# Performance work log

Measured on AMD Instinct MI355X. Metric: run time of the kernel, lower is better.

The kernel has to match this reference:

```python
import jax, jax.numpy as jnp
import numpy as np

B, L, D_MODEL, COND = 2, 2048, 1024, 1024
D_STATE, EXPAND = 64, 2
D_INNER = EXPAND * D_MODEL
MLP_H = 2 * D_MODEL  # mlp_expansion=2
EPS = 1e-5


def setup_inputs() -> dict:
    key = jax.random.key(0)
    ks = jax.random.split(key, 24)
    p = lambda i, shape, s=0.02: (jax.random.normal(ks[i], shape, jnp.float32) * s)
    inp = {
        "x": jax.random.normal(ks[0], (B, L, D_MODEL), jnp.float32),
        "c": jax.random.normal(ks[1], (B, COND), jnp.float32),
        "adaln_mamba_w": p(2, (COND, 3 * D_MODEL)),
        "adaln_mamba_b": jnp.zeros((3 * D_MODEL,), jnp.float32),
        "adaln_mlp_w": p(3, (COND, 3 * D_MODEL)),
        "adaln_mlp_b": jnp.zeros((3 * D_MODEL,), jnp.float32),
        "mlp_w1": p(4, (D_MODEL, MLP_H)),
        "mlp_w2": p(5, (D_MODEL, MLP_H)),
        "mlp_w3": p(6, (MLP_H, D_MODEL)),
    }
    a_init = jnp.log(jnp.tile(jnp.arange(1, D_STATE + 1, dtype=jnp.float32), (D_INNER, 1)))
    for j, pre in enumerate(["fwd", "bwd"]):
        o = 7 + 6 * j
        inp[f"{pre}_in_w"] = p(o, (D_MODEL, 2 * D_INNER))
        inp[f"{pre}_xproj_w"] = p(o + 1, (D_INNER, D_INNER + 2 * D_STATE))
        inp[f"{pre}_dt_bias"] = jnp.zeros((D_INNER,), jnp.float32)
        inp[f"{pre}_A_log"] = a_init
        inp[f"{pre}_D"] = jnp.ones((D_INNER,), jnp.float32)
        inp[f"{pre}_out_w"] = p(o + 2, (D_INNER, D_MODEL))
    return inp


def _adaln(x, c, w, b):
    mod = (c @ w + b)[:, None, :]  # (B,1,3D)
    shift, scale, gate = jnp.split(mod, 3, axis=-1)
    mu = jnp.mean(x, axis=-1, keepdims=True)
    var = jnp.var(x, axis=-1, keepdims=True)
    normed = (x - mu) * jax.lax.rsqrt(var + EPS) * (1.0 + scale) + shift
    return normed, gate


def _ssm(h, in_w, xproj_w, dt_bias, A_log, Dskip, out_w):
    """Selective-SSM: h (B,L,D) -> (B,L,D)."""
    xz = h @ in_w                      # (B,L,2*di)
    xs, z = jnp.split(xz, 2, axis=-1)
    xs = jax.nn.silu(xs)               # (B,L,di)
    proj = xs @ xproj_w                # (B,L,di+2*ds)
    dt = jax.nn.softplus(proj[..., :D_INNER] + dt_bias)        # (B,L,di)
    Bm = proj[..., D_INNER:D_INNER + D_STATE]                  # (B,L,ds)
    Cm = proj[..., D_INNER + D_STATE:]                         # (B,L,ds)
    A = -jnp.exp(A_log)                                        # (di,ds)

    def step(hst, ins):
        dt_t, B_t, C_t, x_t = ins  # (B,di),(B,ds),(B,ds),(B,di)
        dA = jnp.exp(dt_t[:, :, None] * A)                     # (B,di,ds)
        hst = hst * dA + (dt_t * x_t)[:, :, None] * B_t[:, None, :]
        y_t = jnp.einsum('bds,bs->bd', hst, C_t)
        return hst, y_t

    tm = lambda a: jnp.swapaxes(a, 0, 1)  # time-major
    h0 = jnp.zeros((h.shape[0], D_INNER, D_STATE), h.dtype)
    _, ys = jax.lax.scan(step, h0, (tm(dt), tm(Bm), tm(Cm), tm(xs)))
    y = jnp.swapaxes(ys, 0, 1) + xs * Dskip
    return (y * jax.nn.silu(z)) @ out_w


def reference(x, c, adaln_mamba_w, adaln_mamba_b, adaln_mlp_w, adaln_mlp_b,
              mlp_w1, mlp_w2, mlp_w3,
              fwd_in_w, fwd_xproj_w, fwd_dt_bias, fwd_A_log, fwd_D, fwd_out_w,
              bwd_in_w, bwd_xproj_w, bwd_dt_bias, bwd_A_log, bwd_D, bwd_out_w):
    h, gate = _adaln(x, c, adaln_mamba_w, adaln_mamba_b)
    h_fwd = _ssm(h, fwd_in_w, fwd_xproj_w, fwd_dt_bias, fwd_A_log, fwd_D, fwd_out_w)
    h_bwd = jnp.flip(_ssm(jnp.flip(h, 1), bwd_in_w, bwd_xproj_w, bwd_dt_bias, bwd_A_log, bwd_D, bwd_out_w), 1)
    x = x + gate * (h_fwd + h_bwd)
    h, gate = _adaln(x, c, adaln_mlp_w, adaln_mlp_b)
    mlp_out = (jax.nn.silu(h @ mlp_w1) * (h @ mlp_w2)) @ mlp_w3
    return x + gate * mlp_out
```

## Files before the change

### kernel.cpp

```cpp
#include <hip/hip_runtime.h>
#include <hip/hip_bf16.h>
#include <math.h>

#define B_SZ 2
#define LSEQ 2048
#define DM   1024
#define DI   2048
#define NTOK (B_SZ*LSEQ)
#define EPSV 1e-5f

typedef __attribute__((ext_vector_type(8))) short short8v;
typedef __attribute__((ext_vector_type(4))) short short4v;
typedef __attribute__((ext_vector_type(4))) float f4v;

static __device__ __forceinline__ float sigmoidf_(float v) {
    return 1.f / (1.f + __expf(-v));
}
static __device__ __forceinline__ float softplus_(float v) {
    return fmaxf(v, 0.f) + log1pf(__expf(-fabsf(v)));
}
static __device__ __forceinline__ short f2bf(float f) {
    __hip_bfloat16 h = __float2bfloat16(f);
    return *reinterpret_cast<short*>(&h);
}
static __device__ __forceinline__ float bf2f(short s) {
    union { unsigned u; float f; } c;
    c.u = ((unsigned)(unsigned short)s) << 16;
    return c.f;
}

__global__ __launch_bounds__(256) void mod_kernel(const float* __restrict__ c,
                                                  const float* __restrict__ w,
                                                  const float* __restrict__ bias,
                                                  float* __restrict__ mod) {
    int jt = blockIdx.x * 32;
    int jj = threadIdx.x & 31, ks = threadIdx.x >> 5;
    int j = jt + jj;
    const float* c0 = c;
    const float* c1 = c + 1024;
    float a0 = 0.f, a1 = 0.f;
    int k0 = ks * 128;
#pragma unroll 4
    for (int k = k0; k < k0 + 128; ++k) {
        float wv = w[(size_t)k * 3072 + j];
        a0 = fmaf(c0[k], wv, a0);
        a1 = fmaf(c1[k], wv, a1);
    }
    __shared__ float red[2][8][32];
    red[0][ks][jj] = a0;
    red[1][ks][jj] = a1;
    __syncthreads();
    if (threadIdx.x < 64) {
        int bb = threadIdx.x >> 5, j2 = threadIdx.x & 31;
        float s = bias[jt + j2];
#pragma unroll
        for (int kk = 0; kk < 8; ++kk) s += red[bb][kk][j2];
        mod[bb * 3072 + jt + j2] = s;
    }
}

__global__ __launch_bounds__(256) void adaln_kernel(const float* __restrict__ x,
                                                    const float* __restrict__ mod,
                                                    __hip_bfloat16* __restrict__ h) {
    int row = blockIdx.x;
    int b = row >> 11;
    const float* xr = x + (size_t)row * DM;
    float v[4], s = 0.f, s2 = 0.f;
#pragma unroll
    for (int i = 0; i < 4; ++i) {
        v[i] = xr[threadIdx.x + i * 256];
        s += v[i]; s2 += v[i] * v[i];
    }
#pragma unroll
    for (int off = 32; off; off >>= 1) { s += __shfl_xor(s, off); s2 += __shfl_xor(s2, off); }
    __shared__ float red[8];
    int wid = threadIdx.x >> 6;
    if ((threadIdx.x & 63) == 0) { red[wid] = s; red[4 + wid] = s2; }
    __syncthreads();
    s  = red[0] + red[1] + red[2] + red[3];
    s2 = red[4] + red[5] + red[6] + red[7];
    float mu  = s * (1.f / DM);
    float var = s2 * (1.f / DM) - mu * mu;
    float rstd = rsqrtf(var + EPSV);
    const float* mb = mod + b * 3072;
    __hip_bfloat16* hr = h + (size_t)row * DM;
#pragma unroll
    for (int i = 0; i < 4; ++i) {
        int d = threadIdx.x + i * 256;
        hr[d] = __float2bfloat16((v[i] - mu) * rstd * (1.f + mb[1024 + d]) + mb[d]);
    }
}

template <int ACCUM>
__global__ __launch_bounds__(256) void gemm_bf16_kernel(
    const short* __restrict__ A, int lda,
    const short* __restrict__ Bt, int ldb,
    float* __restrict__ C, int ldc, int K)
{
    __shared__ short As[128][40];
    __shared__ short Bs[128][40];
    int tid = threadIdx.x;
    int m0 = blockIdx.y * 128, n0 = blockIdx.x * 128;
    int wave = tid >> 6, lane = tid & 63;
    int wm = (wave & 1) * 64, wn = (wave >> 1) * 64;
    int srow = tid >> 2, sq = (tid & 3) * 8;
    const short* aptr = A + (size_t)(m0 + srow) * lda + sq;
    const short* bptr = Bt + (size_t)(n0 + srow) * ldb + sq;
    int fr = lane & 15, fq = lane >> 4;
    f4v acc[4][4];
#pragma unroll
    for (int i = 0; i < 4; ++i)
#pragma unroll
        for (int j = 0; j < 4; ++j) acc[i][j] = (f4v){0.f, 0.f, 0.f, 0.f};

    short8v a0 = *(const short8v*)(aptr);
    short8v a1 = *(const short8v*)(aptr + 64 * (size_t)lda);
    short8v b0 = *(const short8v*)(bptr);
    short8v b1 = *(const short8v*)(bptr + 64 * (size_t)ldb);
    for (int k0 = 0; k0 < K; k0 += 32) {
        __syncthreads();
        *(short8v*)&As[srow][sq]      = a0;
        *(short8v*)&As[srow + 64][sq] = a1;
        *(short8v*)&Bs[srow][sq]      = b0;
        *(short8v*)&Bs[srow + 64][sq] = b1;
        __syncthreads();
        if (k0 + 32 < K) {
            a0 = *(const short8v*)(aptr + k0 + 32);
            a1 = *(const short8v*)(aptr + 64 * (size_t)lda + k0 + 32);
            b0 = *(const short8v*)(bptr + k0 + 32);
            b1 = *(const short8v*)(bptr + 64 * (size_t)ldb + k0 + 32);
        }
        short8v af[4], bf[4];
#pragma unroll
        for (int i = 0; i < 4; ++i) af[i] = *(const short8v*)&As[wm + i * 16 + fr][fq * 8];
#pragma unroll
        for (int j = 0; j < 4; ++j) bf[j] = *(const short8v*)&Bs[wn + j * 16 + fr][fq * 8];
#pragma unroll
        for (int i = 0; i < 4; ++i)
#pragma unroll
            for (int j = 0; j < 4; ++j)
                acc[i][j] = __builtin_amdgcn_mfma_f32_16x16x32_bf16(af[i], bf[j], acc[i][j], 0, 0, 0);
    }
#pragma unroll
    for (int i = 0; i < 4; ++i)
#pragma unroll
        for (int j = 0; j < 4; ++j) {
#pragma unroll
            for (int r = 0; r < 4; ++r) {
                int row = m0 + wm + i * 16 + fq * 4 + r;
                int col = n0 + wn + j * 16 + fr;
                float* cp = C + (size_t)row * ldc + col;
                if (ACCUM) *cp += acc[i][j][r]; else *cp = acc[i][j][r];
            }
        }
}

__global__ __launch_bounds__(256) void wcast_kernel(const float* __restrict__ w,
                                                    int K, int N,
                                                    short* __restrict__ wT) {
    __shared__ short tile[32][33];
    int c0 = blockIdx.x * 32, r0 = blockIdx.y * 32;
    int tx = threadIdx.x & 31, ty = threadIdx.x >> 5;
#pragma unroll
    for (int i = 0; i < 32; i += 8)
        tile[ty + i][tx] = f2bf(w[(size_t)(r0 + ty + i) * N + c0 + tx]);
    __syncthreads();
#pragma unroll
    for (int i = 0; i < 32; i += 8)
        wT[(size_t)(c0 + ty + i) * K + r0 + tx] = tile[tx][ty + i];
}

__global__ void silu_xs_kernel(float* __restrict__ xz, __hip_bfloat16* __restrict__ xsb) {
    int idx = blockIdx.x * 256 + threadIdx.x;
    int row = idx >> 9, c = (idx & 511) << 2;
    float4* p = (float4*)(xz + (size_t)row * 4096 + c);
    float4 v = *p;
    v.x *= sigmoidf_(v.x); v.y *= sigmoidf_(v.y);
    v.z *= sigmoidf_(v.z); v.w *= sigmoidf_(v.w);
    *p = v;
    short4v s = {f2bf(v.x), f2bf(v.y), f2bf(v.z), f2bf(v.w)};
    *(short4v*)((short*)xsb + (size_t)row * 2048 + c) = s;
}

__global__ __launch_bounds__(256) void transpose_inplace_kernel(float* __restrict__ M) {
    int bj = blockIdx.x, bi = blockIdx.y;
    if (bi > bj) return;
    __shared__ float ta[32][33], tb[32][33];
    int tx = threadIdx.x & 31, ty = threadIdx.x >> 5;
    size_t oA = ((size_t)bi * 32) * 4096 + (size_t)bj * 32;
    size_t oB = ((size_t)bj * 32) * 4096 + (size_t)bi * 32;
#pragma unroll
    for (int i = 0; i < 32; i += 8)
        ta[ty + i][tx] = M[oA + (size_t)(ty + i) * 4096 + tx];
    if (bi != bj) {
#pragma unroll
        for (int i = 0; i < 32; i += 8)
            tb[ty + i][tx] = M[oB + (size_t)(ty + i) * 4096 + tx];
    }
    __syncthreads();
#pragma unroll
    for (int i = 0; i < 32; i += 8)
        M[oB + (size_t)(ty + i) * 4096 + tx] = ta[tx][ty + i];
    if (bi != bj) {
#pragma unroll
        for (int i = 0; i < 32; i += 8)
            M[oA + (size_t)(ty + i) * 4096 + tx] = tb[tx][ty + i];
    }
}

__global__ __launch_bounds__(256) void transpose_dt_kernel(const float* __restrict__ proj,
                                                           const float* __restrict__ bias,
                                                           short* __restrict__ dtT) {
    __shared__ short tile[32][33];
    int c0 = blockIdx.x * 32, r0 = blockIdx.y * 32;
    int tx = threadIdx.x & 31, ty = threadIdx.x >> 5;
#pragma unroll
    for (int i = 0; i < 32; i += 8) {
        float v = proj[(size_t)(r0 + ty + i) * 2176 + c0 + tx];
        tile[ty + i][tx] = f2bf(softplus_(v + bias[c0 + tx]));
    }
    __syncthreads();
#pragma unroll
    for (int i = 0; i < 32; i += 8)
        dtT[(size_t)(c0 + ty + i) * 4096 + r0 + tx] = tile[tx][ty + i];
}

__global__ __launch_bounds__(256) void transpose_bf16_kernel(const short* __restrict__ in,
                                                             short* __restrict__ outp) {
    __shared__ short tile[32][33];
    int c0 = blockIdx.x * 32, r0 = blockIdx.y * 32;
    int tx = threadIdx.x & 31, ty = threadIdx.x >> 5;
#pragma unroll
    for (int i = 0; i < 32; i += 8)
        tile[ty + i][tx] = in[(size_t)(r0 + ty + i) * 4096 + c0 + tx];
    __syncthreads();
#pragma unroll
    for (int i = 0; i < 32; i += 8)
        outp[(size_t)(c0 + ty + i) * 2048 + r0 + tx] = tile[tx][ty + i];
}

#define SLOAD(ib, s0_) {                                                 \
    int sc_ = (s0_) > (LSEQ - 8) ? (LSEQ - 8) : (s0_);                   \
    int bs_ = REV ? (LSEQ - 8) - sc_ : sc_;                              \
    short8v dtv_ = *(const short8v*)(sdt + bs_);                         \
    float4 xv0_ = *(const float4*)(sxs + bs_);                           \
    float4 xv1_ = *(const float4*)(sxs + bs_ + 4);                       \
    _Pragma("unroll")                                                    \
    for (int i_ = 0; i_ < 8; ++i_) {                                     \
        int j_ = REV ? 7 - i_ : i_;                                      \
        dts[ib][i_] = bf2f(dtv_[j_]);                                    \
        xss[ib][i_] = j_ < 4 ? ((const float*)&xv0_)[j_]                 \
                             : ((const float*)&xv1_)[j_ - 4];            \
        int sl_ = sc_ + i_;                                              \
        int tm_ = REV ? (LSEQ - 1) - sl_ : sl_;                          \
        const float* pr_ = projb + (size_t)tm_ * 2176;                   \
        Bbuf[ib][i_] = pr_[2048 + lane];                                 \
        Cbuf[ib][i_] = pr_[2112 + lane];                                 \
    } }

#define SCOMP(ib, r0_)                                                   \
    _Pragma("unroll")                                                    \
    for (int i_ = 0; i_ < 8; ++i_) {                                     \
        float e_ = __builtin_amdgcn_exp2f(dts[ib][i_] * Ae);             \
        float u_ = dts[ib][i_] * xss[ib][i_];                            \
        hst = fmaf(hst, e_, u_ * Bbuf[ib][i_]);                          \
        Lw[((r0_) + i_) * 65] = hst * Cbuf[ib][i_];                      \
    }

template <int REV>
__global__ __launch_bounds__(256) void scan_kernel(
    const float* __restrict__ proj,
    const __hip_bfloat16* __restrict__ dtTp,
    const float* __restrict__ xzT,
    const float* __restrict__ A_log, const float* __restrict__ Dsk,
    __hip_bfloat16* __restrict__ yT)
{
    __shared__ float lds[4][32 * 65];
    int lane = threadIdx.x & 63;
    int wv4 = threadIdx.x >> 6;
    int wave = blockIdx.x * 4 + wv4;
    int b = __builtin_amdgcn_readfirstlane(wave >> 11);
    int d = __builtin_amdgcn_readfirstlane(wave & 2047);
    float A  = -__expf(A_log[d * 64 + lane]);
    float Ae = A * 1.44269504f;
    float Dv = Dsk[d];
    const float* projb = proj + (size_t)b * LSEQ * 2176;
    const short* sdt = (const short*)dtTp + (size_t)d * 4096 + b * 2048;
    const float* sxs = xzT + (size_t)d * 4096 + b * 2048;
    const float* szz = xzT + (size_t)(2048 + d) * 4096 + b * 2048;
    __hip_bfloat16* yrow = yT + (size_t)d * 4096 + b * 2048;
    float* Lw = &lds[wv4][0] + lane;
    const float* Lr = &lds[wv4][0] + (lane & 31) * 65 + (lane >> 5) * 32;
    float hst = 0.f;

    float dts[2][8], xss[2][8], Bbuf[2][8], Cbuf[2][8];
    SLOAD(0, 0);
    for (int s0 = 0; s0 < LSEQ; s0 += 32) {
        SLOAD(1, s0 + 8);  SCOMP(0, 0);
        SLOAD(0, s0 + 16); SCOMP(1, 8);
        SLOAD(1, s0 + 24); SCOMP(0, 16);
        SLOAD(0, s0 + 32); SCOMP(1, 24);
        float ssum = 0.f;
#pragma unroll
        for (int k = 0; k < 32; ++k) ssum += Lr[k];
        ssum += __shfl_xor(ssum, 32);
        if (lane < 32) {
            int tm = REV ? (LSEQ - 1) - (s0 + lane) : (s0 + lane);
            float xv = sxs[tm];
            float zv = szz[tm];
            yrow[tm] = __float2bfloat16(fmaf(xv, Dv, ssum) * (zv * sigmoidf_(zv)));
        }
    }
}

__global__ void gated_add_kernel(const float* __restrict__ x, const float* __restrict__ v,
                                 const float* __restrict__ mod, float* __restrict__ out) {
    int idx = blockIdx.x * 256 + threadIdx.x;
    int row = idx >> 8, b = row >> 11, c = (idx & 255) << 2;
    size_t o = (size_t)row * 1024 + c;
    float4 xv = *(const float4*)(x + o);
    float4 hv = *(const float4*)(v + o);
    float4 gv = *(const float4*)(mod + b * 3072 + 2048 + c);
    float4 r = {fmaf(gv.x, hv.x, xv.x), fmaf(gv.y, hv.y, xv.y),
                fmaf(gv.z, hv.z, xv.z), fmaf(gv.w, hv.w, xv.w)};
    *(float4*)(out + o) = r;
}

__global__ void silumul_kernel(const float* __restrict__ a, const float* __restrict__ bb,
                               __hip_bfloat16* __restrict__ g) {
    int idx = blockIdx.x * 256 + threadIdx.x;
    size_t o = (size_t)idx << 2;
    float4 av = *(const float4*)(a + o);
    float4 bv = *(const float4*)(bb + o);
    short4v r = {f2bf(av.x * sigmoidf_(av.x) * bv.x), f2bf(av.y * sigmoidf_(av.y) * bv.y),
                 f2bf(av.z * sigmoidf_(av.z) * bv.z), f2bf(av.w * sigmoidf_(av.w) * bv.w)};
    *(short4v*)((short*)g + o) = r;
}

extern "C" void kernel_launch(void* const* d_in, const int* in_sizes, int n_in,
                              void* d_out, int out_size, void* d_ws, size_t ws_size,
                              hipStream_t stream) {
    const float* x         = (const float*)d_in[0];
    const float* c         = (const float*)d_in[1];
    const float* adw_mamba = (const float*)d_in[2];
    const float* adb_mamba = (const float*)d_in[3];
    const float* adw_mlp   = (const float*)d_in[4];
    const float* adb_mlp   = (const float*)d_in[5];
    const float* mlp_w1    = (const float*)d_in[6];
    const float* mlp_w2    = (const float*)d_in[7];
    const float* mlp_w3    = (const float*)d_in[8];
    const float* in_w[2]    = {(const float*)d_in[9],  (const float*)d_in[15]};
    const float* xproj_w[2] = {(const float*)d_in[10], (const float*)d_in[16]};
    const float* dt_bias[2] = {(const float*)d_in[11], (const float*)d_in[17]};
    const float* A_log[2]   = {(const float*)d_in[12], (const float*)d_in[18]};
    const float* Dsk[2]     = {(const float*)d_in[13], (const float*)d_in[19]};
    const float* out_w[2]   = {(const float*)d_in[14], (const float*)d_in[20]};
    float* out = (float*)d_out;

    float* ws    = (float*)d_ws;
    float* mod   = ws;
    short* h_bf  = (short*)(ws + 12288);
    float* xz    = ws + 12288 + 2097152;
    float* proj  = xz + 16777216;
    float* scr   = proj + 8912896;
    short* xs_bf = (short*)scr;
    short* dtT   = (short*)scr;
    short* ybtok = (short*)scr;
    short* yTb   = (short*)(scr + 4194304);
    float* hsum  = scr + 8388608;
    short* wb    = (short*)(hsum + 4194304);
    short* inw_b[2]  = {wb,            wb + 4194304};
    short* xpj_b[2]  = {wb + 8388608,  wb + 12845056};
    short* outw_b[2] = {wb + 17301504, wb + 19398656};
    short* w1_b = wb + 21495808;
    short* w2_b = wb + 23592960;
    short* w3_b = wb + 25690112;

    dim3 blk(256);

    for (int dir = 0; dir < 2; ++dir) {
        wcast_kernel<<<dim3(128, 32), blk, 0, stream>>>(in_w[dir],   1024, 4096, inw_b[dir]);
        wcast_kernel<<<dim3(68, 64),  blk, 0, stream>>>(xproj_w[dir],2048, 2176, xpj_b[dir]);
        wcast_kernel<<<dim3(32, 64),  blk, 0, stream>>>(out_w[dir],  2048, 1024, outw_b[dir]);
    }
    wcast_kernel<<<dim3(64, 32), blk, 0, stream>>>(mlp_w1, 1024, 2048, w1_b);
    wcast_kernel<<<dim3(64, 32), blk, 0, stream>>>(mlp_w2, 1024, 2048, w2_b);
    wcast_kernel<<<dim3(32, 64), blk, 0, stream>>>(mlp_w3, 2048, 1024, w3_b);

    mod_kernel<<<96, blk, 0, stream>>>(c, adw_mamba, adb_mamba, mod);
    mod_kernel<<<96, blk, 0, stream>>>(c, adw_mlp,   adb_mlp,   mod + 6144);
    adaln_kernel<<<NTOK, blk, 0, stream>>>(x, mod, (__hip_bfloat16*)h_bf);

    for (int dir = 0; dir < 2; ++dir) {
        gemm_bf16_kernel<0><<<dim3(32, 32), blk, 0, stream>>>(h_bf, 1024, inw_b[dir], 1024, xz, 4096, 1024);
        silu_xs_kernel<<<8192, blk, 0, stream>>>(xz, (__hip_bfloat16*)xs_bf);
        gemm_bf16_kernel<0><<<dim3(17, 32), blk, 0, stream>>>(xs_bf, 2048, xpj_b[dir], 2048, proj, 2176, 2048);
        transpose_inplace_kernel<<<dim3(128, 128), blk, 0, stream>>>(xz);
        transpose_dt_kernel<<<dim3(64, 128), blk, 0, stream>>>(proj, dt_bias[dir], dtT);
        if (dir == 0)
            scan_kernel<0><<<1024, blk, 0, stream>>>(proj, (const __hip_bfloat16*)dtT, xz,
                                                     A_log[dir], Dsk[dir], (__hip_bfloat16*)yTb);
        else
            scan_kernel<1><<<1024, blk, 0, stream>>>(proj, (const __hip_bfloat16*)dtT, xz,
                                                     A_log[dir], Dsk[dir], (__hip_bfloat16*)yTb);
        transpose_bf16_kernel<<<dim3(128, 64), blk, 0, stream>>>(yTb, ybtok);
        if (dir == 0)
            gemm_bf16_kernel<0><<<dim3(8, 32), blk, 0, stream>>>(ybtok, 2048, outw_b[dir], 2048, hsum, 1024, 2048);
        else
            gemm_bf16_kernel<1><<<dim3(8, 32), blk, 0, stream>>>(ybtok, 2048, outw_b[dir], 2048, hsum, 1024, 2048);
    }

    gated_add_kernel<<<4096, blk, 0, stream>>>(x, hsum, mod, out);
    adaln_kernel<<<NTOK, blk, 0, stream>>>(out, mod + 6144, (__hip_bfloat16*)h_bf);
    gemm_bf16_kernel<0><<<dim3(16, 32), blk, 0, stream>>>(h_bf, 1024, w1_b, 1024, xz, 2048, 1024);
    gemm_bf16_kernel<0><<<dim3(16, 32), blk, 0, stream>>>(h_bf, 1024, w2_b, 1024, xz + (size_t)NTOK * 2048, 2048, 1024);
    silumul_kernel<<<8192, blk, 0, stream>>>(xz, xz + (size_t)NTOK * 2048, (__hip_bfloat16*)yTb);
    gemm_bf16_kernel<0><<<dim3(8, 32), blk, 0, stream>>>(yTb, 2048, w3_b, 2048, hsum, 1024, 2048);
    gated_add_kernel<<<4096, blk, 0, stream>>>(out, hsum, mod + 6144, out);
}
```

Measured before the change: 1.247 ms.

## Fuse silu into transpose, gated-add into adaLN, and MLP w1/w2 GEMMs

Folds the SiLU and the bf16 cast of xs into the in-place transpose kernel, so the separate elementwise pass over xz disappears. The residual gated add is merged with the second adaLN, and the two MLP up-projection GEMMs become one wider GEMM over concatenated weights. The aim is fewer full passes over large activations and fewer launches. The fused transpose writes xs_bf with strided per-element stores and must finish before the xproj GEMM, which changes the order of those steps.

Measured after the change: 1.228 ms. About the same (-1.5%).

```diff
diff --git a/kernel.cpp b/kernel.cpp
--- a/kernel.cpp
+++ b/kernel.cpp
@@ -88,6 +88,44 @@
     for (int i = 0; i < 4; ++i) {
         int d = threadIdx.x + i * 256;
         hr[d] = __float2bfloat16((v[i] - mu) * rstd * (1.f + mb[1024 + d]) + mb[d]);
+    }
+}
+
+__global__ __launch_bounds__(256) void gated_adaln_kernel(const float* __restrict__ x,
+                                                          const float* __restrict__ v,
+                                                          const float* __restrict__ modg,
+                                                          const float* __restrict__ modln,
+                                                          float* __restrict__ out,
+                                                          __hip_bfloat16* __restrict__ h) {
+    int row = blockIdx.x;
+    int b = row >> 11;
+    size_t o0 = (size_t)row * DM;
+    float val[4], s = 0.f, s2 = 0.f;
+    const float* gb = modg + b * 3072 + 2048;
+#pragma unroll
+    for (int i = 0; i < 4; ++i) {
+        int d = threadIdx.x + i * 256;
+        val[i] = fmaf(gb[d], v[o0 + d], x[o0 + d]);
+        out[o0 + d] = val[i];
+        s += val[i]; s2 += val[i] * val[i];
+    }
+#pragma unroll
+    for (int off = 32; off; off >>= 1) { s += __shfl_xor(s, off); s2 += __shfl_xor(s2, off); }
+    __shared__ float red[8];
+    int wid = threadIdx.x >> 6;
+    if ((threadIdx.x & 63) == 0) { red[wid] = s; red[4 + wid] = s2; }
+    __syncthreads();
+    s  = red[0] + red[1] + red[2] + red[3];
+    s2 = red[4] + red[5] + red[6] + red[7];
+    float mu  = s * (1.f / DM);
+    float var = s2 * (1.f / DM) - mu * mu;
+    float rstd = rsqrtf(var + EPSV);
+    const float* mb = modln + b * 3072;
+    __hip_bfloat16* hr = h + o0;
+#pragma unroll
+    for (int i = 0; i < 4; ++i) {
+        int d = threadIdx.x + i * 256;
+        hr[d] = __float2bfloat16((val[i] - mu) * rstd * (1.f + mb[1024 + d]) + mb[d]);
     }
 }
 
@@ -170,32 +208,35 @@
         wT[(size_t)(c0 + ty + i) * K + r0 + tx] = tile[tx][ty + i];
 }
 
-__global__ void silu_xs_kernel(float* __restrict__ xz, __hip_bfloat16* __restrict__ xsb) {
-    int idx = blockIdx.x * 256 + threadIdx.x;
-    int row = idx >> 9, c = (idx & 511) << 2;
-    float4* p = (float4*)(xz + (size_t)row * 4096 + c);
-    float4 v = *p;
-    v.x *= sigmoidf_(v.x); v.y *= sigmoidf_(v.y);
-    v.z *= sigmoidf_(v.z); v.w *= sigmoidf_(v.w);
-    *p = v;
-    short4v s = {f2bf(v.x), f2bf(v.y), f2bf(v.z), f2bf(v.w)};
-    *(short4v*)((short*)xsb + (size_t)row * 2048 + c) = s;
-}
-
-__global__ __launch_bounds__(256) void transpose_inplace_kernel(float* __restrict__ M) {
+__global__ __launch_bounds__(256) void silu_transpose_kernel(float* __restrict__ M,
+                                                             short* __restrict__ xsb) {
     int bj = blockIdx.x, bi = blockIdx.y;
     if (bi > bj) return;
     __shared__ float ta[32][33], tb[32][33];
     int tx = threadIdx.x & 31, ty = threadIdx.x >> 5;
     size_t oA = ((size_t)bi * 32) * 4096 + (size_t)bj * 32;
     size_t oB = ((size_t)bj * 32) * 4096 + (size_t)bi * 32;
-#pragma unroll
-    for (int i = 0; i < 32; i += 8)
-        ta[ty + i][tx] = M[oA + (size_t)(ty + i) * 4096 + tx];
+    bool xsA = (bj < 64);
+    bool xsB = (bi < 64);
+#pragma unroll
+    for (int i = 0; i < 32; i += 8) {
+        float v = M[oA + (size_t)(ty + i) * 4096 + tx];
+        if (xsA) {
+            v *= sigmoidf_(v);
+            xsb[(size_t)(bi * 32 + ty + i) * 2048 + bj * 32 + tx] = f2bf(v);
+        }
+        ta[ty + i][tx] = v;
+    }
     if (bi != bj) {
 #pragma unroll
-        for (int i = 0; i < 32; i += 8)
-            tb[ty + i][tx] = M[oB + (size_t)(ty + i) * 4096 + tx];
+        for (int i = 0; i < 32; i += 8) {
+            float v = M[oB + (size_t)(ty + i) * 4096 + tx];
+            if (xsB) {
+                v *= sigmoidf_(v);
+                xsb[(size_t)(bj * 32 + ty + i) * 2048 + bi * 32 + tx] = f2bf(v);
+            }
+            tb[ty + i][tx] = v;
+        }
     }
     __syncthreads();
 #pragma unroll
@@ -326,15 +367,15 @@
     *(float4*)(out + o) = r;
 }
 
-__global__ void silumul_kernel(const float* __restrict__ a, const float* __restrict__ bb,
-                               __hip_bfloat16* __restrict__ g) {
+__global__ void silumul_kernel(const float* __restrict__ ab, __hip_bfloat16* __restrict__ g) {
     int idx = blockIdx.x * 256 + threadIdx.x;
-    size_t o = (size_t)idx << 2;
-    float4 av = *(const float4*)(a + o);
-    float4 bv = *(const float4*)(bb + o);
+    int row = idx >> 9, c = (idx & 511) << 2;
+    size_t o = (size_t)row * 4096 + c;
+    float4 av = *(const float4*)(ab + o);
+    float4 bv = *(const float4*)(ab + o + 2048);
     short4v r = {f2bf(av.x * sigmoidf_(av.x) * bv.x), f2bf(av.y * sigmoidf_(av.y) * bv.y),
                  f2bf(av.z * sigmoidf_(av.z) * bv.z), f2bf(av.w * sigmoidf_(av.w) * bv.w)};
-    *(short4v*)((short*)g + o) = r;
+    *(short4v*)((short*)g + (size_t)row * 2048 + c) = r;
 }
 
 extern "C" void kernel_launch(void* const* d_in, const int* in_sizes, int n_in,
@@ -372,9 +413,8 @@
     short* inw_b[2]  = {wb,            wb + 4194304};
     short* xpj_b[2]  = {wb + 8388608,  wb + 12845056};
     short* outw_b[2] = {wb + 17301504, wb + 19398656};
-    short* w1_b = wb + 21495808;
-    short* w2_b = wb + 23592960;
-    short* w3_b = wb + 25690112;
+    short* w12_b = wb + 21495808;
+    short* w3_b  = wb + 25690112;
 
     dim3 blk(256);
 
@@ -383,8 +423,8 @@
         wcast_kernel<<<dim3(68, 64),  blk, 0, stream>>>(xproj_w[dir],2048, 2176, xpj_b[dir]);
         wcast_kernel<<<dim3(32, 64),  blk, 0, stream>>>(out_w[dir],  2048, 1024, outw_b[dir]);
     }
-    wcast_kernel<<<dim3(64, 32), blk, 0, stream>>>(mlp_w1, 1024, 2048, w1_b);
-    wcast_kernel<<<dim3(64, 32), blk, 0, stream>>>(mlp_w2, 1024, 2048, w2_b);
+    wcast_kernel<<<dim3(64, 32), blk, 0, stream>>>(mlp_w1, 1024, 2048, w12_b);
+    wcast_kernel<<<dim3(64, 32), blk, 0, stream>>>(mlp_w2, 1024, 2048, w12_b + 2097152);
     wcast_kernel<<<dim3(32, 64), blk, 0, stream>>>(mlp_w3, 2048, 1024, w3_b);
 
     mod_kernel<<<96, blk, 0, stream>>>(c, adw_mamba, adb_mamba, mod);
@@ -393,9 +433,8 @@
 
     for (int dir = 0; dir < 2; ++dir) {
         gemm_bf16_kernel<0><<<dim3(32, 32), blk, 0, stream>>>(h_bf, 1024, inw_b[dir], 1024, xz, 4096, 1024);
-        silu_xs_kernel<<<8192, blk, 0, stream>>>(xz, (__hip_bfloat16*)xs_bf);
+        silu_transpose_kernel<<<dim3(128, 128), blk, 0, stream>>>(xz, xs_bf);
         gemm_bf16_kernel<0><<<dim3(17, 32), blk, 0, stream>>>(xs_bf, 2048, xpj_b[dir], 2048, proj, 2176, 2048);
-        transpose_inplace_kernel<<<dim3(128, 128), blk, 0, stream>>>(xz);
         transpose_dt_kernel<<<dim3(64, 128), blk, 0, stream>>>(proj, dt_bias[dir], dtT);
         if (dir == 0)
             scan_kernel<0><<<1024, blk, 0, stream>>>(proj, (const __hip_bfloat16*)dtT, xz,
@@ -410,11 +449,9 @@
             gemm_bf16_kernel<1><<<dim3(8, 32), blk, 0, stream>>>(ybtok, 2048, outw_b[dir], 2048, hsum, 1024, 2048);
     }
 
-    gated_add_kernel<<<4096, blk, 0, stream>>>(x, hsum, mod, out);
-    adaln_kernel<<<NTOK, blk, 0, stream>>>(out, mod + 6144, (__hip_bfloat16*)h_bf);
-    gemm_bf16_kernel<0><<<dim3(16, 32), blk, 0, stream>>>(h_bf, 1024, w1_b, 1024, xz, 2048, 1024);
-    gemm_bf16_kernel<0><<<dim3(16, 32), blk, 0, stream>>>(h_bf, 1024, w2_b, 1024, xz + (size_t)NTOK * 2048, 2048, 1024);
-    silumul_kernel<<<8192, blk, 0, stream>>>(xz, xz + (size_t)NTOK * 2048, (__hip_bfloat16*)yTb);
+    gated_adaln_kernel<<<NTOK, blk, 0, stream>>>(x, hsum, mod, mod + 6144, out, (__hip_bfloat16*)h_bf);
+    gemm_bf16_kernel<0><<<dim3(32, 32), blk, 0, stream>>>(h_bf, 1024, w12_b, 1024, xz, 4096, 1024);
+    silumul_kernel<<<8192, blk, 0, stream>>>(xz, (__hip_bfloat16*)yTb);
     gemm_bf16_kernel<0><<<dim3(8, 32), blk, 0, stream>>>(yTb, 2048, w3_b, 2048, hsum, 1024, 2048);
     gated_add_kernel<<<4096, blk, 0, stream>>>(out, hsum, mod + 6144, out);
 }
```
